# Optimization experiments

Hardware: AMD Instinct MI355X
Metric: run time of the kernel (lower is better)

Reference implementation:

```python
import jax, jax.numpy as jnp
import numpy as np

IN_DIM = 512

def setup_inputs() -> dict:
    key = jax.random.key(0)
    ks = jax.random.split(key, 7)
    s = 1.0 / np.sqrt(IN_DIM)
    x = jax.random.normal(ks[0], (8, 2048, IN_DIM), dtype=jnp.float32)
    Wq = jax.random.uniform(ks[1], (IN_DIM, IN_DIM), jnp.float32, -s, s)
    bq = jax.random.uniform(ks[2], (IN_DIM,), jnp.float32, -s, s)
    Wk = jax.random.uniform(ks[3], (IN_DIM, IN_DIM), jnp.float32, -s, s)
    bk = jax.random.uniform(ks[4], (IN_DIM,), jnp.float32, -s, s)
    Wv = jax.random.uniform(ks[5], (IN_DIM, IN_DIM), jnp.float32, -s, s)
    bv = jax.random.uniform(ks[6], (IN_DIM,), jnp.float32, -s, s)
    return {"x": x, "Wq": Wq, "bq": bq, "Wk": Wk, "bk": bk, "Wv": Wv, "bv": bv}

def reference(x, Wq, bq, Wk, bk, Wv, bv):
    # Q,K,V projections: torch Linear is x @ W.T + b; Wq here is [out,in]
    q = jnp.einsum('bsc,dc->bsd', x, Wq) + bq
    k = jnp.einsum('bsc,dc->bsd', x, Wk) + bk
    v = jnp.einsum('bsc,dc->bsd', x, Wv) + bv
    energy = jnp.einsum('bqd,bkd->bqk', q, k)  # no scaling, matches source
    attention = jax.nn.softmax(energy, axis=-1)
    out = jnp.einsum('bqk,bkd->bqd', attention, v)
    return out
```

## Files before the change

### kernel.cpp

```cpp
#include <hip/hip_runtime.h>

typedef unsigned short u16;
typedef _Float16 f16;

using half8   = __attribute__((ext_vector_type(8))) _Float16;
using f32x4   = __attribute__((ext_vector_type(4))) float;
using ushort8 = __attribute__((ext_vector_type(8))) unsigned short;
using us4     = __attribute__((ext_vector_type(4))) unsigned short;
using float4v = __attribute__((ext_vector_type(4))) float;

#define B_  8
#define S_  2048
#define D_  512
#define BK  32

__device__ __forceinline__ u16 f2h(float f) {
  f16 h = (f16)f;
  u16 u;
  __builtin_memcpy(&u, &h, 2);
  return u;
}

__device__ __forceinline__ float h2f(u16 h) {
  f16 x;
  __builtin_memcpy(&x, &h, 2);
  return (float)x;
}

__device__ __forceinline__ void stage16(const void* g, void* l) {
  __builtin_amdgcn_global_load_lds((const __attribute__((address_space(1))) void*)g,
                                   (__attribute__((address_space(3))) void*)l,
                                   16, 0, 0);
}

__device__ __forceinline__ void xcd_remap(int& bx, int& by, int& bz) {
  const int lin = ((int)blockIdx.z * (int)gridDim.y + (int)blockIdx.y) * (int)gridDim.x
                  + (int)blockIdx.x;
  const int nwg = (int)gridDim.x * (int)gridDim.y * (int)gridDim.z;
  const int swz = (lin & 7) * (nwg >> 3) + (lin >> 3);
  bx = swz % (int)gridDim.x;
  const int tmp = swz / (int)gridDim.x;
  by = tmp % (int)gridDim.y;
  bz = tmp / (int)gridDim.y;
}

template<int M_REP>
__device__ __forceinline__ void gemm_core256(const u16* __restrict__ A,
                                             const u16* __restrict__ B,
                                             int K, int m0, int n0,
                                             u16* lds, f32x4 acc[M_REP][4]) {
  constexpr int BM      = M_REP * 32;
  constexpr int A_ELEMS = BM * 32;
  constexpr int BUFE    = (BM + 256) * 32;
  constexpr int SA      = BM / 128;

  const int tid  = threadIdx.x;
  const int lane = tid & 63;
  const int wave = tid >> 6;
  const int wr = wave >> 2, wc = wave & 3;
  const int fr   = lane & 15;
  const int fgrp = lane >> 4;

  int sra[2], sca[2], srb[2], scb[2];
  #pragma unroll
  for (int s = 0; s < 2; ++s) {
    const int p    = tid * 16 + s * 8192;
    const int R    = p >> 7;
    const int slot = (p >> 4) & 7;
    const int s0   = slot ^ (R & 7);
    sra[s] = srb[s] = 2 * R + (s0 >> 2);
    sca[s] = scb[s] = (s0 & 3) * 8;
  }

  int offA[M_REP], offB[4];
  #pragma unroll
  for (int m = 0; m < M_REP; ++m) {
    const int ra = wr * (M_REP * 16) + m * 16 + fr;
    const int Ra = ra >> 1;
    offA[m] = Ra * 128 + (((((ra & 1) << 2) | fgrp) ^ (Ra & 7)) << 4);
  }
  #pragma unroll
  for (int n = 0; n < 4; ++n) {
    const int rb = wc * 64 + n * 16 + fr;
    const int Rb = rb >> 1;
    offB[n] = Rb * 128 + (((((rb & 1) << 2) | fgrp) ^ (Rb & 7)) << 4);
  }

  const f32x4 vzero = {0.f, 0.f, 0.f, 0.f};
  #pragma unroll
  for (int m = 0; m < M_REP; ++m)
    #pragma unroll
    for (int n = 0; n < 4; ++n)
      acc[m][n] = vzero;

  const int T = K / BK;

  auto STAGE = [&](int t, u16* buf) {
    #pragma unroll
    for (int s = 0; s < SA; ++s)
      stage16(A + (size_t)(m0 + sra[s]) * K + t * BK + sca[s],
              buf + s * 4096 + wave * 512);
    #pragma unroll
    for (int s = 0; s < 2; ++s)
      stage16(B + (size_t)(n0 + srb[s]) * K + t * BK + scb[s],
              buf + A_ELEMS + s * 4096 + wave * 512);
  };

  STAGE(0, lds);
  STAGE(1, lds + BUFE);
  STAGE(2, lds + 2 * BUFE);

  int t = 0;
#define GEMM_ITER(WN)                                                            \
  {                                                                              \
    asm volatile("s_waitcnt vmcnt(" #WN ")\n\ts_barrier" ::: "memory");          \
    const u16* buf = lds + (t & 3) * BUFE;                                       \
    half8 a[M_REP], b[4];                                                        \
    _Pragma("unroll")                                                            \
    for (int m = 0; m < M_REP; ++m)                                              \
      a[m] = *(const half8*)((const char*)buf + offA[m]);                        \
    _Pragma("unroll")                                                            \
    for (int n = 0; n < 4; ++n)                                                  \
      b[n] = *(const half8*)((const char*)(buf + A_ELEMS) + offB[n]);            \
    if (t + 3 < T) STAGE(t + 3, lds + ((t + 3) & 3) * BUFE);                     \
    __builtin_amdgcn_s_setprio(1);                                               \
    _Pragma("unroll")                                                            \
    for (int m = 0; m < M_REP; ++m)                                              \
      _Pragma("unroll")                                                          \
      for (int n = 0; n < 4; ++n)                                                \
        acc[m][n] = __builtin_amdgcn_mfma_f32_16x16x32_f16(a[m], b[n],           \
                                                           acc[m][n], 0, 0, 0); \
    __builtin_amdgcn_s_setprio(0);                                               \
  }

  if constexpr (SA == 2) {
    for (; t < T - 2; ++t) GEMM_ITER(8)
    GEMM_ITER(4); ++t;
    GEMM_ITER(0);
  } else {
    for (; t < T - 2; ++t) GEMM_ITER(6)
    GEMM_ITER(3); ++t;
    GEMM_ITER(0);
  }
#undef GEMM_ITER
}

__global__ __launch_bounds__(512) void proj_kernel(
    const u16* __restrict__ xh, const u16* __restrict__ Wh,
    const float* __restrict__ bq, const float* __restrict__ bk, const float* __restrict__ bv,
    u16* __restrict__ Qb, u16* __restrict__ Kb, u16* __restrict__ Vt) {
  __shared__ __align__(16) u16 lds[4 * (256 + 256) * 32];
  int bx, by, bz;
  xcd_remap(bx, by, bz);
  const int z  = bz;
  const int m0 = by * 256;
  const int n0 = bx * 256;
  const u16* W = Wh + (size_t)z * D_ * D_;
  const float* bias = (z == 0) ? bq : (z == 1) ? bk : bv;
  f32x4 acc[8][4];
  gemm_core256<8>(xh, W, D_, m0, n0, lds, acc);

  const int lane = threadIdx.x & 63;
  const int wave = threadIdx.x >> 6;
  const int wr = wave >> 2, wc = wave & 3;
  #pragma unroll
  for (int m = 0; m < 8; ++m) {
    const int gr0 = m0 + wr * 128 + m * 16 + ((lane >> 4) << 2);
    #pragma unroll
    for (int n = 0; n < 4; ++n) {
      const int gc = n0 + wc * 64 + n * 16 + (lane & 15);
      const float bb = bias[gc];
      if (z < 2) {
        u16* O = z ? Kb : Qb;
        #pragma unroll
        for (int r = 0; r < 4; ++r)
          O[(size_t)(gr0 + r) * D_ + gc] = f2h(acc[m][n][r] + bb);
      } else {
        const int bidx = gr0 >> 11;
        const int s    = gr0 & 2047;
        us4 p;
        #pragma unroll
        for (int r = 0; r < 4; ++r) p[r] = f2h(acc[m][n][r] + bb);
        *(us4*)(Vt + ((size_t)bidx * D_ + gc) * S_ + s) = p;
      }
    }
  }
}

__global__ __launch_bounds__(512) void qk_kernel(
    const u16* __restrict__ Qb, const u16* __restrict__ Kb, u16* __restrict__ E,
    size_t sA, size_t sE) {
  __shared__ __align__(16) u16 lds[4 * (256 + 256) * 32];
  int bx, by, bz;
  xcd_remap(bx, by, bz);
  const int z  = bz;
  const int m0 = by * 256;
  const int n0 = bx * 256;
  f32x4 acc[8][4];
  gemm_core256<8>(Qb + (size_t)z * sA, Kb + (size_t)z * sA, D_, m0, n0, lds, acc);

  u16* Eb = E + (size_t)z * sE;
  const int lane = threadIdx.x & 63;
  const int wave = threadIdx.x >> 6;
  const int wr = wave >> 2, wc = wave & 3;
  #pragma unroll
  for (int m = 0; m < 8; ++m) {
    const int gr0 = m0 + wr * 128 + m * 16 + ((lane >> 4) << 2);
    #pragma unroll
    for (int n = 0; n < 4; ++n) {
      const int gc = n0 + wc * 64 + n * 16 + (lane & 15);
      #pragma unroll
      for (int r = 0; r < 4; ++r)
        Eb[(size_t)(gr0 + r) * S_ + gc] = f2h(acc[m][n][r]);
    }
  }
}

__global__ __launch_bounds__(256) void softmax_kernel(u16* __restrict__ E) {
  const int row  = blockIdx.x * 4 + (threadIdx.x >> 6);
  const int lane = threadIdx.x & 63;
  u16* R = E + (size_t)row * S_;
  float e[32];
  #pragma unroll
  for (int i = 0; i < 4; ++i) {
    ushort8 v = *(const ushort8*)(R + i * 512 + lane * 8);
    #pragma unroll
    for (int j = 0; j < 8; ++j) e[i * 8 + j] = h2f(v[j]);
  }
  float m = e[0];
  #pragma unroll
  for (int i = 1; i < 32; ++i) m = fmaxf(m, e[i]);
  for (int off = 32; off > 0; off >>= 1) m = fmaxf(m, __shfl_xor(m, off, 64));
  float s = 0.f;
  #pragma unroll
  for (int i = 0; i < 32; ++i) { e[i] = __expf(e[i] - m); s += e[i]; }
  for (int off = 32; off > 0; off >>= 1) s += __shfl_xor(s, off, 64);
  const float inv = 1.f / s;
  #pragma unroll
  for (int i = 0; i < 4; ++i) {
    ushort8 v;
    #pragma unroll
    for (int j = 0; j < 8; ++j) v[j] = f2h(e[i * 8 + j] * inv);
    *(ushort8*)(R + i * 512 + lane * 8) = v;
  }
}

__global__ __launch_bounds__(512) void pv_kernel(
    const u16* __restrict__ P, const u16* __restrict__ Vt, float* __restrict__ out,
    size_t sP, size_t sV, size_t sO) {
  __shared__ __align__(16) u16 lds[4 * (128 + 256) * 32];
  int bx, by, bz;
  xcd_remap(bx, by, bz);
  const int z  = bz;
  const int m0 = by * 128;
  const int n0 = bx * 256;
  f32x4 acc[4][4];
  gemm_core256<4>(P + (size_t)z * sP, Vt + (size_t)z * sV, S_, m0, n0, lds, acc);

  float* Ob = out + (size_t)z * sO;
  const int lane = threadIdx.x & 63;
  const int wave = threadIdx.x >> 6;
  const int wr = wave >> 2, wc = wave & 3;
  #pragma unroll
  for (int m = 0; m < 4; ++m) {
    const int gr0 = m0 + wr * 64 + m * 16 + ((lane >> 4) << 2);
    #pragma unroll
    for (int n = 0; n < 4; ++n) {
      const int gc = n0 + wc * 64 + n * 16 + (lane & 15);
      #pragma unroll
      for (int r = 0; r < 4; ++r)
        Ob[(size_t)(gr0 + r) * D_ + gc] = acc[m][n][r];
    }
  }
}

__global__ __launch_bounds__(256) void cvt_kernel(const float* __restrict__ in,
                                                  u16* __restrict__ out, int n8) {
  const int i = blockIdx.x * 256 + threadIdx.x;
  if (i >= n8) return;
  const float4v a = *(const float4v*)(in + (size_t)i * 8);
  const float4v b = *(const float4v*)(in + (size_t)i * 8 + 4);
  ushort8 o;
  o[0] = f2h(a[0]); o[1] = f2h(a[1]); o[2] = f2h(a[2]); o[3] = f2h(a[3]);
  o[4] = f2h(b[0]); o[5] = f2h(b[1]); o[6] = f2h(b[2]); o[7] = f2h(b[3]);
  *(ushort8*)(out + (size_t)i * 8) = o;
}

__global__ __launch_bounds__(256) void cvt3_kernel(const float* __restrict__ w0,
                                                   const float* __restrict__ w1,
                                                   const float* __restrict__ w2,
                                                   u16* __restrict__ out, int n8) {
  const int i = blockIdx.x * 256 + threadIdx.x;
  if (i >= n8) return;
  const float* in = (blockIdx.y == 0) ? w0 : (blockIdx.y == 1) ? w1 : w2;
  u16* o_ = out + (size_t)blockIdx.y * D_ * D_;
  const float4v a = *(const float4v*)(in + (size_t)i * 8);
  const float4v b = *(const float4v*)(in + (size_t)i * 8 + 4);
  ushort8 o;
  o[0] = f2h(a[0]); o[1] = f2h(a[1]); o[2] = f2h(a[2]); o[3] = f2h(a[3]);
  o[4] = f2h(b[0]); o[5] = f2h(b[1]); o[6] = f2h(b[2]); o[7] = f2h(b[3]);
  *(ushort8*)(o_ + (size_t)i * 8) = o;
}

extern "C" void kernel_launch(void* const* d_in, const int* in_sizes, int n_in,
                              void* d_out, int out_size, void* d_ws, size_t ws_size,
                              hipStream_t stream) {
  (void)in_sizes; (void)n_in; (void)out_size;
  const float* x  = (const float*)d_in[0];
  const float* Wq = (const float*)d_in[1];
  const float* bq = (const float*)d_in[2];
  const float* Wk = (const float*)d_in[3];
  const float* bk = (const float*)d_in[4];
  const float* Wv = (const float*)d_in[5];
  const float* bv = (const float*)d_in[6];
  float* out = (float*)d_out;

  char* ws = (char*)d_ws;
  size_t off = 0;
  auto alloc = [&](size_t bytes) -> char* {
    char* p = ws + off;
    off += (bytes + 255) & ~(size_t)255;
    return p;
  };
  const size_t MS = (size_t)B_ * S_;
  u16* xh = (u16*)alloc(MS * D_ * 2);
  u16* Wh = (u16*)alloc(3ull * D_ * D_ * 2);
  u16* Qb = (u16*)alloc(MS * D_ * 2);
  u16* Kb = (u16*)alloc(MS * D_ * 2);
  u16* Vt = (u16*)alloc(MS * D_ * 2);
  const size_t Efull = (size_t)B_ * S_ * S_ * 2;
  const bool full = ws_size >= off + Efull;
  u16* E = (u16*)alloc(full ? Efull : (size_t)S_ * S_ * 2);

  {
    const int n8 = (int)(MS * D_ / 8);
    cvt_kernel<<<dim3((n8 + 255) / 256), dim3(256), 0, stream>>>(x, xh, n8);
    const int w8 = D_ * D_ / 8;
    cvt3_kernel<<<dim3((w8 + 255) / 256, 3), dim3(256), 0, stream>>>(Wq, Wk, Wv, Wh, w8);
  }

  proj_kernel<<<dim3(D_ / 256, MS / 256, 3), dim3(512), 0, stream>>>(
      xh, Wh, bq, bk, bv, Qb, Kb, Vt);

  if (full) {
    qk_kernel<<<dim3(S_ / 256, S_ / 256, B_), dim3(512), 0, stream>>>(
        Qb, Kb, E, (size_t)S_ * D_, (size_t)S_ * S_);
    softmax_kernel<<<dim3(B_ * S_ / 4), dim3(256), 0, stream>>>(E);
    pv_kernel<<<dim3(D_ / 256, S_ / 128, B_), dim3(512), 0, stream>>>(
        E, Vt, out, (size_t)S_ * S_, (size_t)D_ * S_, (size_t)S_ * D_);
  } else {
    for (int b = 0; b < B_; ++b) {
      qk_kernel<<<dim3(S_ / 256, S_ / 256, 1), dim3(512), 0, stream>>>(
          Qb + (size_t)b * S_ * D_, Kb + (size_t)b * S_ * D_, E, 0, 0);
      softmax_kernel<<<dim3(S_ / 4), dim3(256), 0, stream>>>(E);
      pv_kernel<<<dim3(D_ / 256, S_ / 128, 1), dim3(512), 0, stream>>>(
          E, Vt + (size_t)b * D_ * S_, out + (size_t)b * S_ * D_, 0, 0, 0);
    }
  }
}
```

Measured before the change: 164.6 us.

## Replace GEMM core with 64-wide K step, double buffer and quadrant-interleaved staging

The shared GEMM core now uses a K step of 64 with two LDS buffers instead of 32 with four. Each iteration is split into four MFMA quadrants, and global-to-LDS loads for the tile two steps ahead are issued between them behind extra barriers, aiming to overlap memory traffic with matrix math in the style of an 8-wave ping-pong. The projection kernel's M tile is halved to 128 rows so it launches more blocks, and launch bounds pin one block per CU. The extra barriers and single-block occupancy could cost latency hiding if the interleaving does not keep the MFMA units busy.

```diff
diff --git a/kernel.cpp b/kernel.cpp
--- a/kernel.cpp
+++ b/kernel.cpp
@@ -12,7 +12,6 @@
 #define B_  8
 #define S_  2048
 #define D_  512
-#define BK  32
 
 __device__ __forceinline__ u16 f2h(float f) {
   f16 h = (f16)f;
@@ -45,46 +44,80 @@
 }
 
 template<int M_REP>
-__device__ __forceinline__ void gemm_core256(const u16* __restrict__ A,
-                                             const u16* __restrict__ B,
-                                             int K, int m0, int n0,
-                                             u16* lds, f32x4 acc[M_REP][4]) {
-  constexpr int BM      = M_REP * 32;
-  constexpr int A_ELEMS = BM * 32;
-  constexpr int BUFE    = (BM + 256) * 32;
-  constexpr int SA      = BM / 128;
+__device__ __forceinline__ void core8p(const u16* __restrict__ A,
+                                       const u16* __restrict__ B,
+                                       int K, int m0, int n0,
+                                       u16* lds, f32x4 acc[M_REP][4]) {
+  constexpr int M2   = M_REP / 2;
+  constexpr int BM   = M_REP * 32;
+  constexpr int AIS  = BM * 32;
+  constexpr int BOFF = BM * 64;
+  constexpr int BUFE = BM * 64 + 16384;
+  constexpr int ASL  = BM / 128;
+  constexpr int L    = 2 * ASL + 4;
+  constexpr int QSRA = (BM == 256) ? 32 : 16;
 
   const int tid  = threadIdx.x;
   const int lane = tid & 63;
   const int wave = tid >> 6;
   const int wr = wave >> 2, wc = wave & 3;
-  const int fr   = lane & 15;
-  const int fgrp = lane >> 4;
-
-  int sra[2], sca[2], srb[2], scb[2];
-  #pragma unroll
-  for (int s = 0; s < 2; ++s) {
-    const int p    = tid * 16 + s * 8192;
-    const int R    = p >> 7;
-    const int slot = (p >> 4) & 7;
-    const int s0   = slot ^ (R & 7);
-    sra[s] = srb[s] = 2 * R + (s0 >> 2);
-    sca[s] = scb[s] = (s0 & 3) * 8;
-  }
-
-  int offA[M_REP], offB[4];
-  #pragma unroll
-  for (int m = 0; m < M_REP; ++m) {
-    const int ra = wr * (M_REP * 16) + m * 16 + fr;
-    const int Ra = ra >> 1;
-    offA[m] = Ra * 128 + (((((ra & 1) << 2) | fgrp) ^ (Ra & 7)) << 4);
-  }
-  #pragma unroll
-  for (int n = 0; n < 4; ++n) {
-    const int rb = wc * 64 + n * 16 + fr;
-    const int Rb = rb >> 1;
-    offB[n] = Rb * 128 + (((((rb & 1) << 2) | fgrp) ^ (Rb & 7)) << 4);
-  }
+  const int fr = lane & 15, fgrp = lane >> 4;
+
+  int    dstA[2][ASL];  size_t gA[2][ASL];
+  int    dstB[2][2];    size_t gB[2][2];
+  #pragma unroll
+  for (int q = 0; q < 2; ++q) {
+    #pragma unroll
+    for (int s = 0; s < ASL; ++s) {
+      int ks, jr;
+      if constexpr (ASL == 2) { ks = s; jr = wave * 8; }
+      else                    { ks = wave >> 2; jr = (wave & 3) * 8; }
+      const int R   = (jr / QSRA) * (2 * QSRA) + q * QSRA + (jr % QSRA);
+      const int dst = ks * AIS + R * 64;
+      dstA[q][s] = dst;
+      const int e   = dst + lane * 8;
+      const int ks2 = e / AIS, le = e - ks2 * AIS;
+      const int RR  = le >> 6;
+      const int s0  = ((le >> 3) & 7) ^ (RR & 7);
+      gA[q][s] = (size_t)(m0 + 2 * RR + (s0 >> 2)) * K + ks2 * 32 + (s0 & 3) * 8;
+    }
+    #pragma unroll
+    for (int s = 0; s < 2; ++s) {
+      const int jr  = wave * 8;
+      const int R   = (jr / 16) * 32 + q * 16 + (jr % 16);
+      const int dst = BOFF + s * 8192 + R * 64;
+      dstB[q][s] = dst;
+      const int e   = dst - BOFF + lane * 8;
+      const int ks2 = e / 8192, le = e - ks2 * 8192;
+      const int RR  = le >> 6;
+      const int s0  = ((le >> 3) & 7) ^ (RR & 7);
+      gB[q][s] = (size_t)(n0 + 2 * RR + (s0 >> 2)) * K + ks2 * 32 + (s0 & 3) * 8;
+    }
+  }
+
+  int offA[2][M2][2], offB[2][2][2];
+  #pragma unroll
+  for (int mh = 0; mh < 2; ++mh)
+    #pragma unroll
+    for (int m = 0; m < M2; ++m)
+      #pragma unroll
+      for (int ks = 0; ks < 2; ++ks) {
+        const int ra = wr * (M_REP * 16) + (mh * M2 + m) * 16 + fr;
+        const int Ra = ra >> 1;
+        offA[mh][m][ks] = (ks * AIS + Ra * 64) * 2 +
+                          (((((ra & 1) << 2) | fgrp) ^ (Ra & 7)) << 4);
+      }
+  #pragma unroll
+  for (int nh = 0; nh < 2; ++nh)
+    #pragma unroll
+    for (int n = 0; n < 2; ++n)
+      #pragma unroll
+      for (int ks = 0; ks < 2; ++ks) {
+        const int rb = wc * 64 + (nh * 2 + n) * 16 + fr;
+        const int Rb = rb >> 1;
+        offB[nh][n][ks] = (BOFF + ks * 8192 + Rb * 64) * 2 +
+                          (((((rb & 1) << 2) | fgrp) ^ (Rb & 7)) << 4);
+      }
 
   const f32x4 vzero = {0.f, 0.f, 0.f, 0.f};
   #pragma unroll
@@ -93,79 +126,108 @@
     for (int n = 0; n < 4; ++n)
       acc[m][n] = vzero;
 
-  const int T = K / BK;
-
-  auto STAGE = [&](int t, u16* buf) {
-    #pragma unroll
-    for (int s = 0; s < SA; ++s)
-      stage16(A + (size_t)(m0 + sra[s]) * K + t * BK + sca[s],
-              buf + s * 4096 + wave * 512);
+  const int NT = K >> 6;
+
+  auto stageA = [&](int q, int tt) {
+    u16* bb = lds + (tt & 1) * BUFE;
+    #pragma unroll
+    for (int s = 0; s < ASL; ++s)
+      stage16(A + gA[q][s] + (size_t)tt * 64, bb + dstA[q][s]);
+  };
+  auto stageB = [&](int q, int tt) {
+    u16* bb = lds + (tt & 1) * BUFE;
     #pragma unroll
     for (int s = 0; s < 2; ++s)
-      stage16(B + (size_t)(n0 + srb[s]) * K + t * BK + scb[s],
-              buf + A_ELEMS + s * 4096 + wave * 512);
+      stage16(B + gB[q][s] + (size_t)tt * 64, bb + dstB[q][s]);
   };
 
-  STAGE(0, lds);
-  STAGE(1, lds + BUFE);
-  STAGE(2, lds + 2 * BUFE);
-
-  int t = 0;
-#define GEMM_ITER(WN)                                                            \
-  {                                                                              \
-    asm volatile("s_waitcnt vmcnt(" #WN ")\n\ts_barrier" ::: "memory");          \
-    const u16* buf = lds + (t & 3) * BUFE;                                       \
-    half8 a[M_REP], b[4];                                                        \
+  stageA(0, 0); stageB(0, 0); stageB(1, 0); stageA(1, 0);
+  stageA(0, 1); stageB(0, 1); stageB(1, 1); stageA(1, 1);
+
+  half8 a[M2][2], blo[2][2], bhi[2][2];
+
+#define MFMA_Q(MH, BB, NB)                                                       \
+  __builtin_amdgcn_s_setprio(1);                                                 \
+  _Pragma("unroll")                                                              \
+  for (int m = 0; m < M2; ++m)                                                   \
     _Pragma("unroll")                                                            \
-    for (int m = 0; m < M_REP; ++m)                                              \
-      a[m] = *(const half8*)((const char*)buf + offA[m]);                        \
-    _Pragma("unroll")                                                            \
-    for (int n = 0; n < 4; ++n)                                                  \
-      b[n] = *(const half8*)((const char*)(buf + A_ELEMS) + offB[n]);            \
-    if (t + 3 < T) STAGE(t + 3, lds + ((t + 3) & 3) * BUFE);                     \
-    __builtin_amdgcn_s_setprio(1);                                               \
-    _Pragma("unroll")                                                            \
-    for (int m = 0; m < M_REP; ++m)                                              \
+    for (int n = 0; n < 2; ++n)                                                  \
       _Pragma("unroll")                                                          \
-      for (int n = 0; n < 4; ++n)                                                \
-        acc[m][n] = __builtin_amdgcn_mfma_f32_16x16x32_f16(a[m], b[n],           \
-                                                           acc[m][n], 0, 0, 0); \
-    __builtin_amdgcn_s_setprio(0);                                               \
-  }
-
-  if constexpr (SA == 2) {
-    for (; t < T - 2; ++t) GEMM_ITER(8)
-    GEMM_ITER(4); ++t;
-    GEMM_ITER(0);
-  } else {
-    for (; t < T - 2; ++t) GEMM_ITER(6)
-    GEMM_ITER(3); ++t;
-    GEMM_ITER(0);
-  }
-#undef GEMM_ITER
-}
-
-__global__ __launch_bounds__(512) void proj_kernel(
+      for (int ks = 0; ks < 2; ++ks)                                             \
+        acc[(MH) * M2 + m][(NB) + n] = __builtin_amdgcn_mfma_f32_16x16x32_f16(   \
+            a[m][ks], BB[n][ks], acc[(MH) * M2 + m][(NB) + n], 0, 0, 0);         \
+  __builtin_amdgcn_s_setprio(0);
+
+  for (int t = 0; t < NT; ++t) {
+    const char* rb_ = (const char*)(lds + (t & 1) * BUFE);
+    const int tt = t + 2;
+    const bool st = (tt < NT);
+
+    if (t == NT - 1) asm volatile("s_waitcnt vmcnt(0)\n\ts_barrier" ::: "memory");
+    else if constexpr (L == 8) asm volatile("s_waitcnt vmcnt(8)\n\ts_barrier" ::: "memory");
+    else                       asm volatile("s_waitcnt vmcnt(6)\n\ts_barrier" ::: "memory");
+    #pragma unroll
+    for (int m = 0; m < M2; ++m)
+      #pragma unroll
+      for (int ks = 0; ks < 2; ++ks)
+        a[m][ks] = *(const half8*)(rb_ + offA[0][m][ks]);
+    #pragma unroll
+    for (int n = 0; n < 2; ++n)
+      #pragma unroll
+      for (int ks = 0; ks < 2; ++ks)
+        blo[n][ks] = *(const half8*)(rb_ + offB[0][n][ks]);
+    MFMA_Q(0, blo, 0)
+    asm volatile("s_barrier" ::: "memory");
+
+    #pragma unroll
+    for (int n = 0; n < 2; ++n)
+      #pragma unroll
+      for (int ks = 0; ks < 2; ++ks)
+        bhi[n][ks] = *(const half8*)(rb_ + offB[1][n][ks]);
+    if (st) { stageA(0, tt); stageB(0, tt); }
+    asm volatile("s_barrier" ::: "memory");
+    MFMA_Q(0, bhi, 2)
+    asm volatile("s_barrier" ::: "memory");
+
+    #pragma unroll
+    for (int m = 0; m < M2; ++m)
+      #pragma unroll
+      for (int ks = 0; ks < 2; ++ks)
+        a[m][ks] = *(const half8*)(rb_ + offA[1][m][ks]);
+    if (st) stageB(1, tt);
+    asm volatile("s_barrier" ::: "memory");
+    MFMA_Q(1, bhi, 2)
+    asm volatile("s_barrier" ::: "memory");
+
+    if (st) stageA(1, tt);
+    asm volatile("s_barrier" ::: "memory");
+    MFMA_Q(1, blo, 0)
+    asm volatile("s_barrier" ::: "memory");
+  }
+#undef MFMA_Q
+}
+
+__global__ __launch_bounds__(512, 1) void proj_kernel(
     const u16* __restrict__ xh, const u16* __restrict__ Wh,
     const float* __restrict__ bq, const float* __restrict__ bk, const float* __restrict__ bv,
     u16* __restrict__ Qb, u16* __restrict__ Kb, u16* __restrict__ Vt) {
-  __shared__ __align__(16) u16 lds[4 * (256 + 256) * 32];
+  __shared__ __align__(16) u16 lds[2 * (128 * 64 + 16384)];
   int bx, by, bz;
   xcd_remap(bx, by, bz);
   const int z  = bz;
-  const int m0 = by * 256;
+  const int m0 = by * 128;
   const int n0 = bx * 256;
   const u16* W = Wh + (size_t)z * D_ * D_;
   const float* bias = (z == 0) ? bq : (z == 1) ? bk : bv;
-  f32x4 acc[8][4];
-  gemm_core256<8>(xh, W, D_, m0, n0, lds, acc);
+  f32x4 acc[4][4];
+  core8p<4>(xh, W, D_, m0, n0, lds, acc);
 
   const int lane = threadIdx.x & 63;
   const int wave = threadIdx.x >> 6;
   const int wr = wave >> 2, wc = wave & 3;
   #pragma unroll
-  for (int m = 0; m < 8; ++m) {
-    const int gr0 = m0 + wr * 128 + m * 16 + ((lane >> 4) << 2);
+  for (int m = 0; m < 4; ++m) {
+    const int gr0 = m0 + wr * 64 + m * 16 + ((lane >> 4) << 2);
     #pragma unroll
     for (int n = 0; n < 4; ++n) {
       const int gc = n0 + wc * 64 + n * 16 + (lane & 15);
@@ -187,17 +249,17 @@
   }
 }
 
-__global__ __launch_bounds__(512) void qk_kernel(
+__global__ __launch_bounds__(512, 1) void qk_kernel(
     const u16* __restrict__ Qb, const u16* __restrict__ Kb, u16* __restrict__ E,
     size_t sA, size_t sE) {
-  __shared__ __align__(16) u16 lds[4 * (256 + 256) * 32];
+  __shared__ __align__(16) u16 lds[2 * (256 * 64 + 16384)];
   int bx, by, bz;
   xcd_remap(bx, by, bz);
   const int z  = bz;
   const int m0 = by * 256;
   const int n0 = bx * 256;
   f32x4 acc[8][4];
-  gemm_core256<8>(Qb + (size_t)z * sA, Kb + (size_t)z * sA, D_, m0, n0, lds, acc);
+  core8p<8>(Qb + (size_t)z * sA, Kb + (size_t)z * sA, D_, m0, n0, lds, acc);
 
   u16* Eb = E + (size_t)z * sE;
   const int lane = threadIdx.x & 63;
@@ -245,17 +307,17 @@
   }
 }
 
-__global__ __launch_bounds__(512) void pv_kernel(
+__global__ __launch_bounds__(512, 1) void pv_kernel(
     const u16* __restrict__ P, const u16* __restrict__ Vt, float* __restrict__ out,
     size_t sP, size_t sV, size_t sO) {
-  __shared__ __align__(16) u16 lds[4 * (128 + 256) * 32];
+  __shared__ __align__(16) u16 lds[2 * (128 * 64 + 16384)];
   int bx, by, bz;
   xcd_remap(bx, by, bz);
   const int z  = bz;
   const int m0 = by * 128;
   const int n0 = bx * 256;
   f32x4 acc[4][4];
-  gemm_core256<4>(P + (size_t)z * sP, Vt + (size_t)z * sV, S_, m0, n0, lds, acc);
+  core8p<4>(P + (size_t)z * sP, Vt + (size_t)z * sV, S_, m0, n0, lds, acc);
 
   float* Ob = out + (size_t)z * sO;
   const int lane = threadIdx.x & 63;
@@ -339,7 +401,7 @@
     cvt3_kernel<<<dim3((w8 + 255) / 256, 3), dim3(256), 0, stream>>>(Wq, Wk, Wv, Wh, w8);
   }
 
-  proj_kernel<<<dim3(D_ / 256, MS / 256, 3), dim3(512), 0, stream>>>(
+  proj_kernel<<<dim3(D_ / 256, MS / 128, 3), dim3(512), 0, stream>>>(
       xh, Wh, bq, bk, bv, Qb, Kb, Vt);
 
   if (full) {
```

After: 162.8 us. No clear change (-1.0%).
